# Kernel optimization log

Hardware: AMD Instinct MI355X
Metric: run time of the kernel (lower is better)

## Reference

```python
import jax, jax.numpy as jnp
import numpy as np

K = 5  # kernel_size per dim (dim=2 -> 25 kernels), B-spline degree 1, open spline


def spline_conv(x, edge_index, pseudo, W, root, bias):
    # x: [N, Cin], pseudo: [E, 2] in [0,1], W: [K*K, Cin, Cout]
    N = x.shape[0]
    src, dst = edge_index[0], edge_index[1]
    # Transform node features with every kernel weight once: [N, K*K, Cout]
    xk = jnp.einsum('ni,kio->nko', x, W)
    # Degree-1 open B-spline basis: v = u*(K-1); frac/1-frac weights over 2 knots per dim
    v = pseudo * (K - 1)
    bot = jnp.floor(v)
    frac = v - bot
    bot = bot.astype(jnp.int32)
    msg = jnp.zeros((src.shape[0], W.shape[2]), dtype=x.dtype)
    for s0 in (0, 1):
        for s1 in (0, 1):
            b0 = frac[:, 0] if s0 else (1.0 - frac[:, 0])
            b1 = frac[:, 1] if s1 else (1.0 - frac[:, 1])
            basis = b0 * b1  # [E]
            idx = (jnp.clip(bot[:, 0] + s0, 0, K - 1)
                   + K * jnp.clip(bot[:, 1] + s1, 0, K - 1))  # [E]
            msg = msg + basis[:, None] * xk[src, idx]  # gather [E, Cout]
    # scatter-max aggregation into target nodes; empty nodes -> 0 (PyG convention)
    agg = jax.ops.segment_max(msg, dst, num_segments=N)
    agg = jnp.where(jnp.isfinite(agg), agg, jnp.zeros_like(agg))
    return agg + x @ root + bias


def setup_inputs() -> dict:
    key = jax.random.key(0)
    ks = jax.random.split(key, 8)
    N, E, C = 50000, 1600000, 64
    Cin = C
    s = 1.0 / np.sqrt(25 * Cin)
    return {
        'x': jax.random.normal(ks[0], (N, C), dtype=jnp.float32),
        'edge_index': jax.random.randint(ks[1], (2, E), 0, N, dtype=jnp.int32),
        'edge_attr': jax.random.uniform(ks[2], (E, 2), dtype=jnp.float32),
        'W1': jax.random.normal(ks[3], (25, C, C), dtype=jnp.float32) * s,
        'root1': jax.random.normal(ks[4], (C, C), dtype=jnp.float32) / np.sqrt(C),
        'bias1': jnp.zeros((C,), dtype=jnp.float32),
        'W2': jax.random.normal(ks[5], (25, C, C), dtype=jnp.float32) * s,
        'root2': jax.random.normal(ks[6], (C, C), dtype=jnp.float32) / np.sqrt(C),
        'bias2': jnp.zeros((C,), dtype=jnp.float32),
    }


def reference(x, edge_index, edge_attr, W1, root1, bias1, W2, root2, bias2):
    h = jax.nn.relu(spline_conv(x, edge_index, edge_attr, W1, root1, bias1))
    out = spline_conv(h, edge_index, edge_attr, W2, root2, bias2)
    return out
```

## Files before the change

### kernel.cpp

```cpp
#include <hip/hip_runtime.h>
#include <hip/hip_bf16.h>
#include <math.h>

#define CHANNELS 64
#define KK 25
#define NBLK 26
#define NCOL (NBLK * CHANNELS)
#define NTILES (NCOL / 16)
#define ROWP 2560
#define GROUP_TILES 8
#define GROUP_BYTES (GROUP_TILES * 2048)
#define NGROUPS (NTILES / GROUP_TILES)
#define G_SPLIT 5

typedef __attribute__((ext_vector_type(8))) short bf16x8;
typedef __attribute__((ext_vector_type(4))) float f32x4;
typedef __attribute__((ext_vector_type(2))) float f32x2;
typedef unsigned int u32;

__device__ __forceinline__ u32 f2bfu(float f) {
    u32 u = __float_as_uint(f);
    return (u + 0x7FFFu + ((u >> 16) & 1u)) >> 16;
}
__device__ __forceinline__ short f2bf(float f) { return (short)f2bfu(f); }

__device__ __forceinline__ void async_copy16(const void* g, void* l) {
    __builtin_amdgcn_global_load_lds(
        (const __attribute__((address_space(1))) u32*)g,
        (__attribute__((address_space(3))) u32*)l, 16, 0, 0);
}

template<int N> struct IC { static constexpr int v = N; };
template<int G, int GEND, class F>
__device__ __forceinline__ void unrollg(F f) {
    if constexpr (G < GEND) { f(IC<G>{}); unrollg<G + 1, GEND>(f); }
}

__device__ constexpr int cell_stores(int c) {
    return (c < KK) ? (((c % 5) != 0) ? 4 : 0) : 4;
}
__device__ constexpr int grp_stores(int g) {
    return cell_stores(2 * g) + cell_stores(2 * g + 1);
}


__global__ __launch_bounds__(256) void scan_a(const u32* __restrict__ counts,
                                              u32* __restrict__ bsum, int N) {
    const int t = threadIdx.x;
    const int base = blockIdx.x * 1024 + t * 4;
    uint4 v = make_uint4(0, 0, 0, 0);
    if (base + 3 < N) v = *(const uint4*)(counts + base);
    else {
        if (base < N)     v.x = counts[base];
        if (base + 1 < N) v.y = counts[base + 1];
        if (base + 2 < N) v.z = counts[base + 2];
    }
    u32 s = v.x + v.y + v.z + v.w;
    for (int off = 32; off; off >>= 1) s += __shfl_down(s, off, 64);
    __shared__ u32 red[4];
    if ((t & 63) == 0) red[t >> 6] = s;
    __syncthreads();
    if (t == 0) bsum[blockIdx.x] = red[0] + red[1] + red[2] + red[3];
}

__global__ __launch_bounds__(64) void scan_b(u32* __restrict__ bsum, int nb) {
    const int lane = threadIdx.x;
    u32 run = 0;
    for (int base = 0; base < nb; base += 64) {
        u32 v = (base + lane < nb) ? bsum[base + lane] : 0u;
        const u32 orig = v;
        for (int off = 1; off < 64; off <<= 1) {
            u32 u = __shfl_up(v, off, 64);
            if (lane >= off) v += u;
        }
        if (base + lane < nb) bsum[base + lane] = run + v - orig;
        run += __shfl(v, 63, 64);
    }
}

__global__ __launch_bounds__(256) void scan_c(const u32* __restrict__ counts,
                                              const u32* __restrict__ bsum,
                                              u32* __restrict__ cursor, int N) {
    const int t = threadIdx.x;
    const int base = blockIdx.x * 1024 + t * 4;
    uint4 v = make_uint4(0, 0, 0, 0);
    if (base + 3 < N) v = *(const uint4*)(counts + base);
    else {
        if (base < N)     v.x = counts[base];
        if (base + 1 < N) v.y = counts[base + 1];
        if (base + 2 < N) v.z = counts[base + 2];
    }
    __shared__ u32 ps[256];
    ps[t] = v.x + v.y + v.z + v.w;
    __syncthreads();
    for (int off = 1; off < 256; off <<= 1) {
        u32 u = (t >= off) ? ps[t - off] : 0u;
        __syncthreads();
        ps[t] += u;
        __syncthreads();
    }
    u32 ex = ((t > 0) ? ps[t - 1] : 0u) + bsum[blockIdx.x];
    if (base < N)     cursor[base]     = ex;
    if (base + 1 < N) cursor[base + 1] = ex + v.x;
    if (base + 2 < N) cursor[base + 2] = ex + v.x + v.y;
    if (base + 3 < N) cursor[base + 3] = ex + v.x + v.y + v.z;
    if (base <= N - 1 && N - 1 <= base + 3)
        cursor[N] = ex + v.x + v.y + v.z + v.w;
}


__global__ __launch_bounds__(256) void prep_w(const float* __restrict__ W,
                                              const float* __restrict__ root,
                                              __hip_bfloat16* __restrict__ Wb) {
    int idx = blockIdx.x * 256 + threadIdx.x;
    if (idx >= NTILES * 2 * 64 * 8) return;
    int j = idx & 7;
    int l = (idx >> 3) & 63;
    int q = (idx >> 9) & 1;
    int t = idx >> 10;
    int cell = t >> 2;
    int o    = 4 * (l & 15) + (t & 3);
    int k    = q * 32 + (l >> 4) * 8 + j;
    float src = (cell < KK) ? W[cell * 4096 + k * 64 + o] : root[k * 64 + o];
    ((unsigned short*)Wb)[idx] = (unsigned short)f2bf(src);
}

template<int GR0, int GR1>
__device__ __forceinline__ void gemm_body(
    const float* __restrict__ X, const __hip_bfloat16* __restrict__ Wb,
    char* __restrict__ XK, float* __restrict__ rootf, int N)
{
    static_assert((2 * GR0) % 5 == 0 || 2 * GR0 >= KK, "prevp chain crosses kernel split");
    __shared__ __align__(16) char lds[2][GROUP_BYTES];
    const int lane = threadIdx.x & 63;
    const int wv   = threadIdx.x >> 6;
    const int rb   = blockIdx.x * 64 + wv * 16;
    const int m    = lane & 15;
    const int quad = lane >> 4;
    const int Nm1  = N - 1;

    const int rowc = min(rb + m, Nm1);
    const float* __restrict__ xp = X + (size_t)rowc * CHANNELS + quad * 8;
    float af[16];
    *(float4*)(af)      = *(const float4*)(xp);
    *(float4*)(af + 4)  = *(const float4*)(xp + 4);
    *(float4*)(af + 8)  = *(const float4*)(xp + 32);
    *(float4*)(af + 12) = *(const float4*)(xp + 36);
    bf16x8 A0, A1;
#pragma unroll
    for (int j = 0; j < 8; ++j) { A0[j] = f2bf(af[j]); A1[j] = f2bf(af[8 + j]); }

    const int r0 = rb + quad * 4;
    const char* __restrict__ wbc = (const char*)Wb;

    auto stage = [&](int gg, int buf) {
        const char* gsrc = wbc + (size_t)gg * GROUP_BYTES + wv * 4096 + lane * 16;
        char* lbase = lds[buf] + wv * 4096;
        async_copy16(gsrc,        lbase);
        async_copy16(gsrc + 1024, lbase + 1024);
        async_copy16(gsrc + 2048, lbase + 2048);
        async_copy16(gsrc + 3072, lbase + 3072);
    };

    u32 prevp[4] = {0u, 0u, 0u, 0u};

    stage(GR0, 0);

    unrollg<GR0, GR1>([&](auto icg) {
        constexpr int g = decltype(icg)::v;
        constexpr int K = (g == GR0) ? 0 : grp_stores(g - 1);
        asm volatile("s_waitcnt vmcnt(%0)" :: "i"(K) : "memory");
        asm volatile("s_waitcnt lgkmcnt(0)" ::: "memory");
        __builtin_amdgcn_s_barrier();
        __builtin_amdgcn_sched_barrier(0);
        if constexpr (g + 1 < GR1) stage(g + 1, (g + 1 - GR0) & 1);
        __builtin_amdgcn_sched_barrier(0);
        const char* lb = lds[(g - GR0) & 1] + lane * 16;

        auto cell = [&](auto ick, const char* cb) {
            constexpr int kc = decltype(ick)::v;
            f32x4 acc0 = {0.f, 0.f, 0.f, 0.f};
            f32x4 acc1 = {0.f, 0.f, 0.f, 0.f};
            f32x4 acc2 = {0.f, 0.f, 0.f, 0.f};
            f32x4 acc3 = {0.f, 0.f, 0.f, 0.f};
            acc0 = __builtin_amdgcn_mfma_f32_16x16x32_bf16(A0, *(const bf16x8*)(cb),        acc0, 0, 0, 0);
            acc0 = __builtin_amdgcn_mfma_f32_16x16x32_bf16(A1, *(const bf16x8*)(cb + 1024), acc0, 0, 0, 0);
            acc1 = __builtin_amdgcn_mfma_f32_16x16x32_bf16(A0, *(const bf16x8*)(cb + 2048), acc1, 0, 0, 0);
            acc1 = __builtin_amdgcn_mfma_f32_16x16x32_bf16(A1, *(const bf16x8*)(cb + 3072), acc1, 0, 0, 0);
            acc2 = __builtin_amdgcn_mfma_f32_16x16x32_bf16(A0, *(const bf16x8*)(cb + 4096), acc2, 0, 0, 0);
            acc2 = __builtin_amdgcn_mfma_f32_16x16x32_bf16(A1, *(const bf16x8*)(cb + 5120), acc2, 0, 0, 0);
            acc3 = __builtin_amdgcn_mfma_f32_16x16x32_bf16(A0, *(const bf16x8*)(cb + 6144), acc3, 0, 0, 0);
            acc3 = __builtin_amdgcn_mfma_f32_16x16x32_bf16(A1, *(const bf16x8*)(cb + 7168), acc3, 0, 0, 0);
            if constexpr (kc < KK) {
                constexpr int d1 = kc / 5;
                constexpr int d0 = kc % 5;
                u32 pk[4];
#pragma unroll
                for (int i = 0; i < 4; ++i) {
                    u32 p = __builtin_amdgcn_cvt_pk_fp8_f32(acc0[i], acc1[i], 0u, false);
                    p = __builtin_amdgcn_cvt_pk_fp8_f32(acc2[i], acc3[i], p, true);
                    pk[i] = p;
                }
                if constexpr (d0 >= 1) {
#pragma unroll
                    for (int i = 0; i < 4; ++i) {
                        const int r = min(r0 + i, Nm1);
                        *(uint2*)(XK + (size_t)r * ROWP
                                  + (d1 * 512 + (d0 - 1) * 128) + 8 * m) =
                            make_uint2(prevp[i], pk[i]);
                    }
                }
#pragma unroll
                for (int i = 0; i < 4; ++i) prevp[i] = pk[i];
            } else {
#pragma unroll
                for (int i = 0; i < 4; ++i) {
                    const int r = min(r0 + i, Nm1);
                    *(float4*)(rootf + (size_t)r * CHANNELS + 4 * m) =
                        make_float4(acc0[i], acc1[i], acc2[i], acc3[i]);
                }
            }
        };
        cell(IC<2 * g>{},     lb);
        cell(IC<2 * g + 1>{}, lb + 8192);
    });
}

__global__ __launch_bounds__(256) void gemm_hist(
    const float* __restrict__ X, const __hip_bfloat16* __restrict__ Wb,
    char* __restrict__ XK, float* __restrict__ rootf, int N, int gemm_blocks,
    const int* __restrict__ ei, u32* __restrict__ counts,
    u32* __restrict__ rank, int E)
{
    if ((int)blockIdx.x >= gemm_blocks) {
        const int e0 = ((int)blockIdx.x - gemm_blocks) * 1024 + threadIdx.x * 4;
        if (e0 + 3 < E) {
            const int4 d = *(const int4*)(ei + E + e0);
            const u32 r0 = atomicAdd(&counts[d.x], 1u);
            const u32 r1 = atomicAdd(&counts[d.y], 1u);
            const u32 r2 = atomicAdd(&counts[d.z], 1u);
            const u32 r3 = atomicAdd(&counts[d.w], 1u);
            *(uint4*)(rank + e0) = make_uint4(r0, r1, r2, r3);
        } else {
            for (int k = 0; k < 4; ++k)
                if (e0 + k < E)
                    rank[e0 + k] = atomicAdd(&counts[ei[E + e0 + k]], 1u);
        }
        return;
    }
    gemm_body<0, G_SPLIT>(X, Wb, XK, rootf, N);
}

__device__ __forceinline__ uint2 mkrec(int src, float v0f, float v1f) {
    const float v0 = v0f * 4.0f, v1 = v1f * 4.0f;
    const int p0 = max(min((int)floorf(v0), 3), 0);
    const int p1 = max(min((int)floorf(v1), 3), 0);
    const float f0 = v0 - (float)p0;
    const float f1 = v1 - (float)p1;
    const u32 f0q = min((u32)(f0 * 65536.0f), 65535u);
    const u32 f1q = min((u32)(f1 * 65536.0f), 65535u);
    uint2 rec;
    rec.x = (u32)src | ((u32)p0 << 16) | ((u32)p1 << 19);
    rec.y = f0q | (f1q << 16);
    return rec;
}

__global__ __launch_bounds__(256) void gemm_scatter(
    const float* __restrict__ X, const __hip_bfloat16* __restrict__ Wb,
    char* __restrict__ XK, float* __restrict__ rootf, int N, int gemm_blocks,
    const int* __restrict__ ei, const float* __restrict__ ps,
    const u32* __restrict__ rank, const u32* __restrict__ cursor,
    uint2* __restrict__ sorted, int E)
{
    if ((int)blockIdx.x >= gemm_blocks) {
        const int e0 = ((int)blockIdx.x - gemm_blocks) * 1024 + threadIdx.x * 4;
        if (e0 + 3 < E) {
            const int4 s  = *(const int4*)(ei + e0);
            const int4 d  = *(const int4*)(ei + E + e0);
            const float4 pa = *(const float4*)(ps + 2 * e0);
            const float4 pb = *(const float4*)(ps + 2 * e0 + 4);
            const uint4 rk = *(const uint4*)(rank + e0);
            const u32 c0 = cursor[d.x];
            const u32 c1 = cursor[d.y];
            const u32 c2 = cursor[d.z];
            const u32 c3 = cursor[d.w];
            sorted[c0 + rk.x] = mkrec(s.x, pa.x, pa.y);
            sorted[c1 + rk.y] = mkrec(s.y, pa.z, pa.w);
            sorted[c2 + rk.z] = mkrec(s.z, pb.x, pb.y);
            sorted[c3 + rk.w] = mkrec(s.w, pb.z, pb.w);
        } else {
            for (int k = 0; k < 4; ++k) {
                const int e = e0 + k;
                if (e < E)
                    sorted[cursor[ei[E + e]] + rank[e]] =
                        mkrec(ei[e], ps[2 * e], ps[2 * e + 1]);
            }
        }
        return;
    }
    gemm_body<G_SPLIT, NGROUPS>(X, Wb, XK, rootf, N);
}

__global__ __launch_bounds__(256) void gemm_only(
    const float* __restrict__ X, const __hip_bfloat16* __restrict__ Wb,
    char* __restrict__ XK, float* __restrict__ rootf, int N)
{
    gemm_body<0, NGROUPS>(X, Wb, XK, rootf, N);
}

__global__ __launch_bounds__(256) void agg_node_p(
    const uint2* __restrict__ sorted, const u32* __restrict__ cursor,
    const char* __restrict__ XK, const float* __restrict__ rootf,
    const float* __restrict__ bias, float* __restrict__ out, int N, int relu,
    int node_blocks, const float* __restrict__ Wsrc,
    const float* __restrict__ rootsrc, __hip_bfloat16* __restrict__ Wbdst)
{
    if ((int)blockIdx.x >= node_blocks) {
        int idx = ((int)blockIdx.x - node_blocks) * 256 + threadIdx.x;
        if (idx < NTILES * 2 * 64 * 8) {
            int j = idx & 7;
            int l = (idx >> 3) & 63;
            int q = (idx >> 9) & 1;
            int t = idx >> 10;
            int cell = t >> 2;
            int o    = 4 * (l & 15) + (t & 3);
            int k    = q * 32 + (l >> 4) * 8 + j;
            float s = (cell < KK) ? Wsrc[cell * 4096 + k * 64 + o] : rootsrc[k * 64 + o];
            ((unsigned short*)Wbdst)[idx] = (unsigned short)f2bf(s);
        }
        return;
    }
    const int lane = threadIdx.x & 63;
    const int n = blockIdx.x * 4 + (threadIdx.x >> 6);
    if (n >= N) return;
    const int q = lane >> 4, j = lane & 15;
    const int beg = (int)cursor[n];
    const int end = (int)cursor[n + 1];

    float m0 = -INFINITY, m1 = -INFINITY, m2 = -INFINITY, m3 = -INFINITY;
    if (beg < end) {
        const int last = end - 1;
#define GATHP(r, q0, q1)                                                       \
        {                                                                      \
            const char* b_ = XK + (size_t)((r).x & 0xffff) * ROWP + (j << 3);  \
            const int o_ = (((int)((r).x >> 16) & 7)                           \
                            + (((int)((r).x >> 19) & 7) << 2)) << 7;           \
            q0 = *(const uint2*)(b_ + o_);                                     \
            q1 = *(const uint2*)(b_ + o_ + 512);                               \
        }
        uint2 rA = sorted[min(beg + q,      last)];
        uint2 rB = sorted[min(beg + 4 + q,  last)];
        uint2 rC = sorted[min(beg + 8 + q,  last)];
        uint2 ga0, ga1, gb0, gb1, gc0, gc1;
        GATHP(rA, ga0, ga1)
        GATHP(rB, gb0, gb1)
        for (int i = beg; i < end; i += 4) {
            uint2 rD = sorted[min(i + 12 + q, last)];
            GATHP(rC, gc0, gc1)
            const float f0 = (float)(rA.y & 0xffff) * (1.0f / 65536.0f);
            const float f1 = (float)(rA.y >> 16)    * (1.0f / 65536.0f);
            const float w00 = (1.f - f0) * (1.f - f1);
            const float w10 = f0 * (1.f - f1);
            const float w01 = (1.f - f0) * f1;
            const float w11 = f0 * f1;
            f32x2 s01 = __builtin_amdgcn_cvt_pk_f32_fp8(ga0.x, false) * w00
                      + __builtin_amdgcn_cvt_pk_f32_fp8(ga0.y, false) * w10
                      + __builtin_amdgcn_cvt_pk_f32_fp8(ga1.x, false) * w01
                      + __builtin_amdgcn_cvt_pk_f32_fp8(ga1.y, false) * w11;
            f32x2 s23 = __builtin_amdgcn_cvt_pk_f32_fp8(ga0.x, true)  * w00
                      + __builtin_amdgcn_cvt_pk_f32_fp8(ga0.y, true)  * w10
                      + __builtin_amdgcn_cvt_pk_f32_fp8(ga1.x, true)  * w01
                      + __builtin_amdgcn_cvt_pk_f32_fp8(ga1.y, true)  * w11;
            m0 = fmaxf(m0, s01.x); m1 = fmaxf(m1, s01.y);
            m2 = fmaxf(m2, s23.x); m3 = fmaxf(m3, s23.y);
            rA = rB; rB = rC; rC = rD;
            ga0 = gb0; ga1 = gb1;
            gb0 = gc0; gb1 = gc1;
        }
#undef GATHP
    }
    m0 = fmaxf(m0, __shfl_xor(m0, 16, 64)); m0 = fmaxf(m0, __shfl_xor(m0, 32, 64));
    m1 = fmaxf(m1, __shfl_xor(m1, 16, 64)); m1 = fmaxf(m1, __shfl_xor(m1, 32, 64));
    m2 = fmaxf(m2, __shfl_xor(m2, 16, 64)); m2 = fmaxf(m2, __shfl_xor(m2, 32, 64));
    m3 = fmaxf(m3, __shfl_xor(m3, 16, 64)); m3 = fmaxf(m3, __shfl_xor(m3, 32, 64));
    const float a0 = isfinite(m0) ? m0 : 0.f;
    const float a1 = isfinite(m1) ? m1 : 0.f;
    const float a2 = isfinite(m2) ? m2 : 0.f;
    const float a3 = isfinite(m3) ? m3 : 0.f;

    const float4 rv = *(const float4*)(rootf + (size_t)n * CHANNELS + 4 * j);
    const float4 bv = *(const float4*)(bias + 4 * j);
    float r0 = a0 + rv.x + bv.x;
    float r1 = a1 + rv.y + bv.y;
    float r2 = a2 + rv.z + bv.z;
    float r3 = a3 + rv.w + bv.w;
    if (relu) {
        r0 = fmaxf(r0, 0.f); r1 = fmaxf(r1, 0.f);
        r2 = fmaxf(r2, 0.f); r3 = fmaxf(r3, 0.f);
    }
    if (q == 0)
        *(float4*)(out + (size_t)n * CHANNELS + 4 * j) = make_float4(r0, r1, r2, r3);
}

extern "C" void kernel_launch(void* const* d_in, const int* in_sizes, int n_in,
                              void* d_out, int out_size, void* d_ws, size_t ws_size,
                              hipStream_t stream) {
    const float* x     = (const float*)d_in[0];
    const int*   ei    = (const int*)d_in[1];
    const float* ps    = (const float*)d_in[2];
    const float* W1    = (const float*)d_in[3];
    const float* root1 = (const float*)d_in[4];
    const float* bias1 = (const float*)d_in[5];
    const float* W2    = (const float*)d_in[6];
    const float* root2 = (const float*)d_in[7];
    const float* bias2 = (const float*)d_in[8];
    float* out = (float*)d_out;

    const int N = in_sizes[0] / CHANNELS;
    const int E = in_sizes[1] / 2;

    char* ws = (char*)d_ws;
    char* xk = ws;
    size_t off = (size_t)N * ROWP;
    float* h = (float*)(ws + off);
    off += (size_t)N * CHANNELS * sizeof(float);
    float* rootf = (float*)(ws + off);
    off += (size_t)N * CHANNELS * sizeof(float);
    uint2* sorted = (uint2*)(ws + off);
    off += (size_t)E * sizeof(uint2);
    u32* rank = (u32*)(ws + off);
    off += (size_t)E * sizeof(u32);
    u32* counts = (u32*)(ws + off);
    off += (size_t)N * 4;
    __hip_bfloat16* Wb = (__hip_bfloat16*)(ws + off);
    off += (size_t)NTILES * 2 * 64 * 8 * 2;
    u32* cursor = (u32*)(ws + off);
    off += ((size_t)N + 1) * 4;
    u32* bsum = (u32*)(ws + off);

    const int prep_blocks = (NTILES * 2 * 64 * 8 + 255) / 256;
    const int gemm_blocks = (N + 63) / 64;
    const int node_blocks = (N + 3) / 4;
    const int edgeQ_blocks = (E + 1023) / 1024;
    const int scan_blocks = (N + 1023) / 1024;

    hipMemsetAsync(counts, 0, (size_t)N * 4, stream);
    prep_w<<<prep_blocks, 256, 0, stream>>>(W1, root1, Wb);

    gemm_hist<<<gemm_blocks + edgeQ_blocks, 256, 0, stream>>>(
        x, Wb, xk, rootf, N, gemm_blocks, ei, counts, rank, E);

    scan_a<<<scan_blocks, 256, 0, stream>>>(counts, bsum, N);
    scan_b<<<1, 64, 0, stream>>>(bsum, scan_blocks);
    scan_c<<<scan_blocks, 256, 0, stream>>>(counts, bsum, cursor, N);

    gemm_scatter<<<gemm_blocks + edgeQ_blocks, 256, 0, stream>>>(
        x, Wb, xk, rootf, N, gemm_blocks, ei, ps, rank, cursor, sorted, E);

    agg_node_p<<<node_blocks + prep_blocks, 256, 0, stream>>>(
        sorted, cursor, xk, rootf, bias1, h, N, 1, node_blocks, W2, root2, Wb);

    gemm_only<<<gemm_blocks, 256, 0, stream>>>(h, Wb, xk, rootf, N);
    agg_node_p<<<node_blocks, 256, 0, stream>>>(
        sorted, cursor, xk, rootf, bias2, out, N, 0, node_blocks, W2, root2, Wb);
}
```

Baseline: 416.6 us.

## Unfuse GEMM from edge sort, use atomic cursor scatter and nontemporal stores

The layer-1 GEMM is no longer split across the histogram and scatter kernels. It runs as its own kernel, with nontemporal stores for the transformed features. The histogram becomes a standalone kernel that only counts and no longer records per-edge ranks. The scatter now claims slots with atomic increments on a live copy of the cursor, which removes the rank array's write and read traffic. The cost is losing the overlap between edge sorting and GEMM, and the order of edges within each node becomes nondeterministic; that order is harmless for max aggregation.

```diff
diff --git a/kernel.cpp b/kernel.cpp
--- a/kernel.cpp
+++ b/kernel.cpp
@@ -11,12 +11,13 @@
 #define GROUP_TILES 8
 #define GROUP_BYTES (GROUP_TILES * 2048)
 #define NGROUPS (NTILES / GROUP_TILES)
-#define G_SPLIT 5
 
 typedef __attribute__((ext_vector_type(8))) short bf16x8;
 typedef __attribute__((ext_vector_type(4))) float f32x4;
 typedef __attribute__((ext_vector_type(2))) float f32x2;
 typedef unsigned int u32;
+typedef __attribute__((ext_vector_type(2))) unsigned int u32x2;
+typedef __attribute__((ext_vector_type(4))) float f32x4v;
 
 __device__ __forceinline__ u32 f2bfu(float f) {
     u32 u = __float_as_uint(f);
@@ -80,7 +81,8 @@
 
 __global__ __launch_bounds__(256) void scan_c(const u32* __restrict__ counts,
                                               const u32* __restrict__ bsum,
-                                              u32* __restrict__ cursor, int N) {
+                                              u32* __restrict__ cursor,
+                                              u32* __restrict__ curlive, int N) {
     const int t = threadIdx.x;
     const int base = blockIdx.x * 1024 + t * 4;
     uint4 v = make_uint4(0, 0, 0, 0);
@@ -100,12 +102,27 @@
         __syncthreads();
     }
     u32 ex = ((t > 0) ? ps[t - 1] : 0u) + bsum[blockIdx.x];
-    if (base < N)     cursor[base]     = ex;
-    if (base + 1 < N) cursor[base + 1] = ex + v.x;
-    if (base + 2 < N) cursor[base + 2] = ex + v.x + v.y;
-    if (base + 3 < N) cursor[base + 3] = ex + v.x + v.y + v.z;
+    if (base < N)     { cursor[base]     = ex;                   curlive[base]     = ex; }
+    if (base + 1 < N) { cursor[base + 1] = ex + v.x;             curlive[base + 1] = ex + v.x; }
+    if (base + 2 < N) { cursor[base + 2] = ex + v.x + v.y;       curlive[base + 2] = ex + v.x + v.y; }
+    if (base + 3 < N) { cursor[base + 3] = ex + v.x + v.y + v.z; curlive[base + 3] = ex + v.x + v.y + v.z; }
     if (base <= N - 1 && N - 1 <= base + 3)
         cursor[N] = ex + v.x + v.y + v.z + v.w;
+}
+
+__global__ __launch_bounds__(256) void hist_edges(const int* __restrict__ ei,
+                                                  u32* __restrict__ counts, int E) {
+    const int e0 = blockIdx.x * 1024 + threadIdx.x * 4;
+    if (e0 + 3 < E) {
+        const int4 d = *(const int4*)(ei + E + e0);
+        atomicAdd(&counts[d.x], 1u);
+        atomicAdd(&counts[d.y], 1u);
+        atomicAdd(&counts[d.z], 1u);
+        atomicAdd(&counts[d.w], 1u);
+    } else {
+        for (int k = 0; k < 4; ++k)
+            if (e0 + k < E) atomicAdd(&counts[ei[E + e0 + k]], 1u);
+    }
 }
 
 
@@ -125,12 +142,11 @@
     ((unsigned short*)Wb)[idx] = (unsigned short)f2bf(src);
 }
 
-template<int GR0, int GR1>
+template<int NT>
 __device__ __forceinline__ void gemm_body(
     const float* __restrict__ X, const __hip_bfloat16* __restrict__ Wb,
     char* __restrict__ XK, float* __restrict__ rootf, int N)
 {
-    static_assert((2 * GR0) % 5 == 0 || 2 * GR0 >= KK, "prevp chain crosses kernel split");
     __shared__ __align__(16) char lds[2][GROUP_BYTES];
     const int lane = threadIdx.x & 63;
     const int wv   = threadIdx.x >> 6;
@@ -164,18 +180,18 @@
 
     u32 prevp[4] = {0u, 0u, 0u, 0u};
 
-    stage(GR0, 0);
-
-    unrollg<GR0, GR1>([&](auto icg) {
+    stage(0, 0);
+
+    unrollg<0, NGROUPS>([&](auto icg) {
         constexpr int g = decltype(icg)::v;
-        constexpr int K = (g == GR0) ? 0 : grp_stores(g - 1);
+        constexpr int K = (g == 0) ? 0 : grp_stores(g - 1);
         asm volatile("s_waitcnt vmcnt(%0)" :: "i"(K) : "memory");
         asm volatile("s_waitcnt lgkmcnt(0)" ::: "memory");
         __builtin_amdgcn_s_barrier();
         __builtin_amdgcn_sched_barrier(0);
-        if constexpr (g + 1 < GR1) stage(g + 1, (g + 1 - GR0) & 1);
+        if constexpr (g + 1 < NGROUPS) stage(g + 1, (g + 1) & 1);
         __builtin_amdgcn_sched_barrier(0);
-        const char* lb = lds[(g - GR0) & 1] + lane * 16;
+        const char* lb = lds[g & 1] + lane * 16;
 
         auto cell = [&](auto ick, const char* cb) {
             constexpr int kc = decltype(ick)::v;
@@ -205,9 +221,14 @@
 #pragma unroll
                     for (int i = 0; i < 4; ++i) {
                         const int r = min(r0 + i, Nm1);
-                        *(uint2*)(XK + (size_t)r * ROWP
-                                  + (d1 * 512 + (d0 - 1) * 128) + 8 * m) =
-                            make_uint2(prevp[i], pk[i]);
+                        char* addr = XK + (size_t)r * ROWP
+                                     + (d1 * 512 + (d0 - 1) * 128) + 8 * m;
+                        if constexpr (NT) {
+                            u32x2 v; v.x = prevp[i]; v.y = pk[i];
+                            __builtin_nontemporal_store(v, (u32x2*)addr);
+                        } else {
+                            *(uint2*)addr = make_uint2(prevp[i], pk[i]);
+                        }
                     }
                 }
 #pragma unroll
@@ -216,8 +237,13 @@
 #pragma unroll
                 for (int i = 0; i < 4; ++i) {
                     const int r = min(r0 + i, Nm1);
-                    *(float4*)(rootf + (size_t)r * CHANNELS + 4 * m) =
-                        make_float4(acc0[i], acc1[i], acc2[i], acc3[i]);
+                    float* addr = rootf + (size_t)r * CHANNELS + 4 * m;
+                    if constexpr (NT) {
+                        f32x4v v; v.x = acc0[i]; v.y = acc1[i]; v.z = acc2[i]; v.w = acc3[i];
+                        __builtin_nontemporal_store(v, (f32x4v*)addr);
+                    } else {
+                        *(float4*)addr = make_float4(acc0[i], acc1[i], acc2[i], acc3[i]);
+                    }
                 }
             }
         };
@@ -226,29 +252,12 @@
     });
 }
 
-__global__ __launch_bounds__(256) void gemm_hist(
+template<int NT>
+__global__ __launch_bounds__(256) void gemm_only(
     const float* __restrict__ X, const __hip_bfloat16* __restrict__ Wb,
-    char* __restrict__ XK, float* __restrict__ rootf, int N, int gemm_blocks,
-    const int* __restrict__ ei, u32* __restrict__ counts,
-    u32* __restrict__ rank, int E)
+    char* __restrict__ XK, float* __restrict__ rootf, int N)
 {
-    if ((int)blockIdx.x >= gemm_blocks) {
-        const int e0 = ((int)blockIdx.x - gemm_blocks) * 1024 + threadIdx.x * 4;
-        if (e0 + 3 < E) {
-            const int4 d = *(const int4*)(ei + E + e0);
-            const u32 r0 = atomicAdd(&counts[d.x], 1u);
-            const u32 r1 = atomicAdd(&counts[d.y], 1u);
-            const u32 r2 = atomicAdd(&counts[d.z], 1u);
-            const u32 r3 = atomicAdd(&counts[d.w], 1u);
-            *(uint4*)(rank + e0) = make_uint4(r0, r1, r2, r3);
-        } else {
-            for (int k = 0; k < 4; ++k)
-                if (e0 + k < E)
-                    rank[e0 + k] = atomicAdd(&counts[ei[E + e0 + k]], 1u);
-        }
-        return;
-    }
-    gemm_body<0, G_SPLIT>(X, Wb, XK, rootf, N);
+    gemm_body<NT>(X, Wb, XK, rootf, N);
 }
 
 __device__ __forceinline__ uint2 mkrec(int src, float v0f, float v1f) {
@@ -265,47 +274,33 @@
     return rec;
 }
 
-__global__ __launch_bounds__(256) void gemm_scatter(
-    const float* __restrict__ X, const __hip_bfloat16* __restrict__ Wb,
-    char* __restrict__ XK, float* __restrict__ rootf, int N, int gemm_blocks,
+__global__ __launch_bounds__(256) void edge_scatter(
     const int* __restrict__ ei, const float* __restrict__ ps,
-    const u32* __restrict__ rank, const u32* __restrict__ cursor,
-    uint2* __restrict__ sorted, int E)
+    u32* __restrict__ curlive, uint2* __restrict__ sorted, int E)
 {
-    if ((int)blockIdx.x >= gemm_blocks) {
-        const int e0 = ((int)blockIdx.x - gemm_blocks) * 1024 + threadIdx.x * 4;
-        if (e0 + 3 < E) {
-            const int4 s  = *(const int4*)(ei + e0);
-            const int4 d  = *(const int4*)(ei + E + e0);
-            const float4 pa = *(const float4*)(ps + 2 * e0);
-            const float4 pb = *(const float4*)(ps + 2 * e0 + 4);
-            const uint4 rk = *(const uint4*)(rank + e0);
-            const u32 c0 = cursor[d.x];
-            const u32 c1 = cursor[d.y];
-            const u32 c2 = cursor[d.z];
-            const u32 c3 = cursor[d.w];
-            sorted[c0 + rk.x] = mkrec(s.x, pa.x, pa.y);
-            sorted[c1 + rk.y] = mkrec(s.y, pa.z, pa.w);
-            sorted[c2 + rk.z] = mkrec(s.z, pb.x, pb.y);
-            sorted[c3 + rk.w] = mkrec(s.w, pb.z, pb.w);
-        } else {
-            for (int k = 0; k < 4; ++k) {
-                const int e = e0 + k;
-                if (e < E)
-                    sorted[cursor[ei[E + e]] + rank[e]] =
-                        mkrec(ei[e], ps[2 * e], ps[2 * e + 1]);
+    const int e0 = blockIdx.x * 1024 + threadIdx.x * 4;
+    if (e0 + 3 < E) {
+        const int4 s  = *(const int4*)(ei + e0);
+        const int4 d  = *(const int4*)(ei + E + e0);
+        const float4 pa = *(const float4*)(ps + 2 * e0);
+        const float4 pb = *(const float4*)(ps + 2 * e0 + 4);
+        const u32 c0 = atomicAdd(&curlive[d.x], 1u);
+        const u32 c1 = atomicAdd(&curlive[d.y], 1u);
+        const u32 c2 = atomicAdd(&curlive[d.z], 1u);
+        const u32 c3 = atomicAdd(&curlive[d.w], 1u);
+        sorted[c0] = mkrec(s.x, pa.x, pa.y);
+        sorted[c1] = mkrec(s.y, pa.z, pa.w);
+        sorted[c2] = mkrec(s.z, pb.x, pb.y);
+        sorted[c3] = mkrec(s.w, pb.z, pb.w);
+    } else {
+        for (int k = 0; k < 4; ++k) {
+            const int e = e0 + k;
+            if (e < E) {
+                const u32 c = atomicAdd(&curlive[ei[E + e]], 1u);
+                sorted[c] = mkrec(ei[e], ps[2 * e], ps[2 * e + 1]);
             }
         }
-        return;
-    }
-    gemm_body<G_SPLIT, NGROUPS>(X, Wb, XK, rootf, N);
-}
-
-__global__ __launch_bounds__(256) void gemm_only(
-    const float* __restrict__ X, const __hip_bfloat16* __restrict__ Wb,
-    char* __restrict__ XK, float* __restrict__ rootf, int N)
-{
-    gemm_body<0, NGROUPS>(X, Wb, XK, rootf, N);
+    }
 }
 
 __global__ __launch_bounds__(256) void agg_node_p(
@@ -428,14 +423,14 @@
     off += (size_t)N * CHANNELS * sizeof(float);
     uint2* sorted = (uint2*)(ws + off);
     off += (size_t)E * sizeof(uint2);
-    u32* rank = (u32*)(ws + off);
-    off += (size_t)E * sizeof(u32);
     u32* counts = (u32*)(ws + off);
     off += (size_t)N * 4;
     __hip_bfloat16* Wb = (__hip_bfloat16*)(ws + off);
     off += (size_t)NTILES * 2 * 64 * 8 * 2;
     u32* cursor = (u32*)(ws + off);
     off += ((size_t)N + 1) * 4;
+    u32* curlive = (u32*)(ws + off);
+    off += ((size_t)N + 1) * 4;
     u32* bsum = (u32*)(ws + off);
 
     const int prep_blocks = (NTILES * 2 * 64 * 8 + 255) / 256;
@@ -445,22 +440,23 @@
     const int scan_blocks = (N + 1023) / 1024;
 
     hipMemsetAsync(counts, 0, (size_t)N * 4, stream);
+
+    hist_edges<<<edgeQ_blocks, 256, 0, stream>>>(ei, counts, E);
+
     prep_w<<<prep_blocks, 256, 0, stream>>>(W1, root1, Wb);
 
-    gemm_hist<<<gemm_blocks + edgeQ_blocks, 256, 0, stream>>>(
-        x, Wb, xk, rootf, N, gemm_blocks, ei, counts, rank, E);
+    gemm_only<1><<<gemm_blocks, 256, 0, stream>>>(x, Wb, xk, rootf, N);
 
     scan_a<<<scan_blocks, 256, 0, stream>>>(counts, bsum, N);
     scan_b<<<1, 64, 0, stream>>>(bsum, scan_blocks);
-    scan_c<<<scan_blocks, 256, 0, stream>>>(counts, bsum, cursor, N);
-
-    gemm_scatter<<<gemm_blocks + edgeQ_blocks, 256, 0, stream>>>(
-        x, Wb, xk, rootf, N, gemm_blocks, ei, ps, rank, cursor, sorted, E);
+    scan_c<<<scan_blocks, 256, 0, stream>>>(counts, bsum, cursor, curlive, N);
+
+    edge_scatter<<<edgeQ_blocks, 256, 0, stream>>>(ei, ps, curlive, sorted, E);
 
     agg_node_p<<<node_blocks + prep_blocks, 256, 0, stream>>>(
         sorted, cursor, xk, rootf, bias1, h, N, 1, node_blocks, W2, root2, Wb);
 
-    gemm_only<<<gemm_blocks, 256, 0, stream>>>(h, Wb, xk, rootf, N);
+    gemm_only<0><<<gemm_blocks, 256, 0, stream>>>(h, Wb, xk, rootf, N);
     agg_node_p<<<node_blocks, 256, 0, stream>>>(
         sorted, cursor, xk, rootf, bias2, out, N, 0, node_blocks, W2, root2, Wb);
 }
```

After: 476.4 us. +14.4%, slower.

## Use per-wave private weight staging in GEMM and unfuse edge passes

Applied to the files above, without the earlier changes.

The GEMM kernel now gives each wave its own double-buffered LDS copy of each 8 KB weight cell. This removes the block-wide s_barrier per group, and each wave prefetches two cells ahead using only vmcnt/lgkmcnt waits. The histogram and scatter edge passes are split back out of the fused GEMM launches into standalone kernels, and the GEMM runs as a single full kernel. The barriers go away, but each wave now loads the weights redundantly (4x the global-to-LDS traffic) and uses 64 KB of LDS per block, which may limit occupancy. Splitting the launches also loses the overlap between the edge work and the GEMM.

```diff
diff --git a/kernel.cpp b/kernel.cpp
--- a/kernel.cpp
+++ b/kernel.cpp
@@ -8,10 +8,7 @@
 #define NCOL (NBLK * CHANNELS)
 #define NTILES (NCOL / 16)
 #define ROWP 2560
-#define GROUP_TILES 8
-#define GROUP_BYTES (GROUP_TILES * 2048)
-#define NGROUPS (NTILES / GROUP_TILES)
-#define G_SPLIT 5
+#define CELL_BYTES 8192
 
 typedef __attribute__((ext_vector_type(8))) short bf16x8;
 typedef __attribute__((ext_vector_type(4))) float f32x4;
@@ -38,9 +35,6 @@
 
 __device__ constexpr int cell_stores(int c) {
     return (c < KK) ? (((c % 5) != 0) ? 4 : 0) : 4;
-}
-__device__ constexpr int grp_stores(int g) {
-    return cell_stores(2 * g) + cell_stores(2 * g + 1);
 }
 
 
@@ -106,6 +100,24 @@
     if (base + 3 < N) cursor[base + 3] = ex + v.x + v.y + v.z;
     if (base <= N - 1 && N - 1 <= base + 3)
         cursor[N] = ex + v.x + v.y + v.z + v.w;
+}
+
+__global__ __launch_bounds__(256) void hist_edges(const int* __restrict__ ei,
+                                                  u32* __restrict__ counts,
+                                                  u32* __restrict__ rank, int E) {
+    const int e0 = blockIdx.x * 1024 + threadIdx.x * 4;
+    if (e0 + 3 < E) {
+        const int4 d = *(const int4*)(ei + E + e0);
+        const u32 r0 = atomicAdd(&counts[d.x], 1u);
+        const u32 r1 = atomicAdd(&counts[d.y], 1u);
+        const u32 r2 = atomicAdd(&counts[d.z], 1u);
+        const u32 r3 = atomicAdd(&counts[d.w], 1u);
+        *(uint4*)(rank + e0) = make_uint4(r0, r1, r2, r3);
+    } else {
+        for (int k = 0; k < 4; ++k)
+            if (e0 + k < E)
+                rank[e0 + k] = atomicAdd(&counts[ei[E + e0 + k]], 1u);
+    }
 }
 
 
@@ -125,13 +137,11 @@
     ((unsigned short*)Wb)[idx] = (unsigned short)f2bf(src);
 }
 
-template<int GR0, int GR1>
-__device__ __forceinline__ void gemm_body(
+__global__ __launch_bounds__(256) void gemm_nb(
     const float* __restrict__ X, const __hip_bfloat16* __restrict__ Wb,
     char* __restrict__ XK, float* __restrict__ rootf, int N)
 {
-    static_assert((2 * GR0) % 5 == 0 || 2 * GR0 >= KK, "prevp chain crosses kernel split");
-    __shared__ __align__(16) char lds[2][GROUP_BYTES];
+    __shared__ __align__(16) char lds[4][2][CELL_BYTES];
     const int lane = threadIdx.x & 63;
     const int wv   = threadIdx.x >> 6;
     const int rb   = blockIdx.x * 64 + wv * 16;
@@ -152,103 +162,75 @@
 
     const int r0 = rb + quad * 4;
     const char* __restrict__ wbc = (const char*)Wb;
-
-    auto stage = [&](int gg, int buf) {
-        const char* gsrc = wbc + (size_t)gg * GROUP_BYTES + wv * 4096 + lane * 16;
-        char* lbase = lds[buf] + wv * 4096;
-        async_copy16(gsrc,        lbase);
-        async_copy16(gsrc + 1024, lbase + 1024);
-        async_copy16(gsrc + 2048, lbase + 2048);
-        async_copy16(gsrc + 3072, lbase + 3072);
+    char* const ldsw = &lds[wv][0][0];
+
+    auto stage = [&](int c, int buf) {
+        const char* gsrc = wbc + (size_t)c * CELL_BYTES + lane * 16;
+        char* lb = ldsw + buf * CELL_BYTES;
+#pragma unroll
+        for (int k = 0; k < 8; ++k)
+            async_copy16(gsrc + k * 1024, lb + k * 1024);
     };
 
     u32 prevp[4] = {0u, 0u, 0u, 0u};
 
-    stage(GR0, 0);
-
-    unrollg<GR0, GR1>([&](auto icg) {
-        constexpr int g = decltype(icg)::v;
-        constexpr int K = (g == GR0) ? 0 : grp_stores(g - 1);
-        asm volatile("s_waitcnt vmcnt(%0)" :: "i"(K) : "memory");
-        asm volatile("s_waitcnt lgkmcnt(0)" ::: "memory");
-        __builtin_amdgcn_s_barrier();
-        __builtin_amdgcn_sched_barrier(0);
-        if constexpr (g + 1 < GR1) stage(g + 1, (g + 1 - GR0) & 1);
-        __builtin_amdgcn_sched_barrier(0);
-        const char* lb = lds[(g - GR0) & 1] + lane * 16;
-
-        auto cell = [&](auto ick, const char* cb) {
-            constexpr int kc = decltype(ick)::v;
-            f32x4 acc0 = {0.f, 0.f, 0.f, 0.f};
-            f32x4 acc1 = {0.f, 0.f, 0.f, 0.f};
-            f32x4 acc2 = {0.f, 0.f, 0.f, 0.f};
-            f32x4 acc3 = {0.f, 0.f, 0.f, 0.f};
-            acc0 = __builtin_amdgcn_mfma_f32_16x16x32_bf16(A0, *(const bf16x8*)(cb),        acc0, 0, 0, 0);
-            acc0 = __builtin_amdgcn_mfma_f32_16x16x32_bf16(A1, *(const bf16x8*)(cb + 1024), acc0, 0, 0, 0);
-            acc1 = __builtin_amdgcn_mfma_f32_16x16x32_bf16(A0, *(const bf16x8*)(cb + 2048), acc1, 0, 0, 0);
-            acc1 = __builtin_amdgcn_mfma_f32_16x16x32_bf16(A1, *(const bf16x8*)(cb + 3072), acc1, 0, 0, 0);
-            acc2 = __builtin_amdgcn_mfma_f32_16x16x32_bf16(A0, *(const bf16x8*)(cb + 4096), acc2, 0, 0, 0);
-            acc2 = __builtin_amdgcn_mfma_f32_16x16x32_bf16(A1, *(const bf16x8*)(cb + 5120), acc2, 0, 0, 0);
-            acc3 = __builtin_amdgcn_mfma_f32_16x16x32_bf16(A0, *(const bf16x8*)(cb + 6144), acc3, 0, 0, 0);
-            acc3 = __builtin_amdgcn_mfma_f32_16x16x32_bf16(A1, *(const bf16x8*)(cb + 7168), acc3, 0, 0, 0);
-            if constexpr (kc < KK) {
-                constexpr int d1 = kc / 5;
-                constexpr int d0 = kc % 5;
-                u32 pk[4];
-#pragma unroll
-                for (int i = 0; i < 4; ++i) {
-                    u32 p = __builtin_amdgcn_cvt_pk_fp8_f32(acc0[i], acc1[i], 0u, false);
-                    p = __builtin_amdgcn_cvt_pk_fp8_f32(acc2[i], acc3[i], p, true);
-                    pk[i] = p;
-                }
-                if constexpr (d0 >= 1) {
-#pragma unroll
-                    for (int i = 0; i < 4; ++i) {
-                        const int r = min(r0 + i, Nm1);
-                        *(uint2*)(XK + (size_t)r * ROWP
-                                  + (d1 * 512 + (d0 - 1) * 128) + 8 * m) =
-                            make_uint2(prevp[i], pk[i]);
-                    }
-                }
-#pragma unroll
-                for (int i = 0; i < 4; ++i) prevp[i] = pk[i];
-            } else {
+    stage(0, 0);
+    stage(1, 1);
+
+    unrollg<0, NBLK>([&](auto icc) {
+        constexpr int c = decltype(icc)::v;
+        constexpr int NC = (c == 0) ? 8
+                         : cell_stores(c - 1) + ((c + 1 < NBLK) ? 8 : 0);
+        asm volatile("s_waitcnt vmcnt(%0)" :: "i"(NC) : "memory");
+
+        const char* cb = ldsw + (c & 1) * CELL_BYTES + lane * 16;
+        f32x4 acc0 = {0.f, 0.f, 0.f, 0.f};
+        f32x4 acc1 = {0.f, 0.f, 0.f, 0.f};
+        f32x4 acc2 = {0.f, 0.f, 0.f, 0.f};
+        f32x4 acc3 = {0.f, 0.f, 0.f, 0.f};
+        acc0 = __builtin_amdgcn_mfma_f32_16x16x32_bf16(A0, *(const bf16x8*)(cb),        acc0, 0, 0, 0);
+        acc0 = __builtin_amdgcn_mfma_f32_16x16x32_bf16(A1, *(const bf16x8*)(cb + 1024), acc0, 0, 0, 0);
+        acc1 = __builtin_amdgcn_mfma_f32_16x16x32_bf16(A0, *(const bf16x8*)(cb + 2048), acc1, 0, 0, 0);
+        acc1 = __builtin_amdgcn_mfma_f32_16x16x32_bf16(A1, *(const bf16x8*)(cb + 3072), acc1, 0, 0, 0);
+        acc2 = __builtin_amdgcn_mfma_f32_16x16x32_bf16(A0, *(const bf16x8*)(cb + 4096), acc2, 0, 0, 0);
+        acc2 = __builtin_amdgcn_mfma_f32_16x16x32_bf16(A1, *(const bf16x8*)(cb + 5120), acc2, 0, 0, 0);
+        acc3 = __builtin_amdgcn_mfma_f32_16x16x32_bf16(A0, *(const bf16x8*)(cb + 6144), acc3, 0, 0, 0);
+        acc3 = __builtin_amdgcn_mfma_f32_16x16x32_bf16(A1, *(const bf16x8*)(cb + 7168), acc3, 0, 0, 0);
+
+        if constexpr (c < KK) {
+            constexpr int d1 = c / 5;
+            constexpr int d0 = c % 5;
+            u32 pk[4];
+#pragma unroll
+            for (int i = 0; i < 4; ++i) {
+                u32 p = __builtin_amdgcn_cvt_pk_fp8_f32(acc0[i], acc1[i], 0u, false);
+                p = __builtin_amdgcn_cvt_pk_fp8_f32(acc2[i], acc3[i], p, true);
+                pk[i] = p;
+            }
+            if constexpr (d0 >= 1) {
 #pragma unroll
                 for (int i = 0; i < 4; ++i) {
                     const int r = min(r0 + i, Nm1);
-                    *(float4*)(rootf + (size_t)r * CHANNELS + 4 * m) =
-                        make_float4(acc0[i], acc1[i], acc2[i], acc3[i]);
+                    *(uint2*)(XK + (size_t)r * ROWP
+                              + (d1 * 512 + (d0 - 1) * 128) + 8 * m) =
+                        make_uint2(prevp[i], pk[i]);
                 }
             }
-        };
-        cell(IC<2 * g>{},     lb);
-        cell(IC<2 * g + 1>{}, lb + 8192);
+#pragma unroll
+            for (int i = 0; i < 4; ++i) prevp[i] = pk[i];
+        } else {
+#pragma unroll
+            for (int i = 0; i < 4; ++i) {
+                const int r = min(r0 + i, Nm1);
+                *(float4*)(rootf + (size_t)r * CHANNELS + 4 * m) =
+                    make_float4(acc0[i], acc1[i], acc2[i], acc3[i]);
+            }
+        }
+        if constexpr (c + 2 < NBLK) {
+            asm volatile("s_waitcnt lgkmcnt(0)" ::: "memory");
+            stage(c + 2, c & 1);
+        }
     });
-}
-
-__global__ __launch_bounds__(256) void gemm_hist(
-    const float* __restrict__ X, const __hip_bfloat16* __restrict__ Wb,
-    char* __restrict__ XK, float* __restrict__ rootf, int N, int gemm_blocks,
-    const int* __restrict__ ei, u32* __restrict__ counts,
-    u32* __restrict__ rank, int E)
-{
-    if ((int)blockIdx.x >= gemm_blocks) {
-        const int e0 = ((int)blockIdx.x - gemm_blocks) * 1024 + threadIdx.x * 4;
-        if (e0 + 3 < E) {
-            const int4 d = *(const int4*)(ei + E + e0);
-            const u32 r0 = atomicAdd(&counts[d.x], 1u);
-            const u32 r1 = atomicAdd(&counts[d.y], 1u);
-            const u32 r2 = atomicAdd(&counts[d.z], 1u);
-            const u32 r3 = atomicAdd(&counts[d.w], 1u);
-            *(uint4*)(rank + e0) = make_uint4(r0, r1, r2, r3);
-        } else {
-            for (int k = 0; k < 4; ++k)
-                if (e0 + k < E)
-                    rank[e0 + k] = atomicAdd(&counts[ei[E + e0 + k]], 1u);
-        }
-        return;
-    }
-    gemm_body<0, G_SPLIT>(X, Wb, XK, rootf, N);
 }
 
 __device__ __forceinline__ uint2 mkrec(int src, float v0f, float v1f) {
@@ -265,47 +247,34 @@
     return rec;
 }
 
-__global__ __launch_bounds__(256) void gemm_scatter(
-    const float* __restrict__ X, const __hip_bfloat16* __restrict__ Wb,
-    char* __restrict__ XK, float* __restrict__ rootf, int N, int gemm_blocks,
+__global__ __launch_bounds__(256) void edge_scatter(
     const int* __restrict__ ei, const float* __restrict__ ps,
     const u32* __restrict__ rank, const u32* __restrict__ cursor,
     uint2* __restrict__ sorted, int E)
 {
-    if ((int)blockIdx.x >= gemm_blocks) {
-        const int e0 = ((int)blockIdx.x - gemm_blocks) * 1024 + threadIdx.x * 4;
-        if (e0 + 3 < E) {
-            const int4 s  = *(const int4*)(ei + e0);
-            const int4 d  = *(const int4*)(ei + E + e0);
-            const float4 pa = *(const float4*)(ps + 2 * e0);
-            const float4 pb = *(const float4*)(ps + 2 * e0 + 4);
-            const uint4 rk = *(const uint4*)(rank + e0);
-            const u32 c0 = cursor[d.x];
-            const u32 c1 = cursor[d.y];
-            const u32 c2 = cursor[d.z];
-            const u32 c3 = cursor[d.w];
-            sorted[c0 + rk.x] = mkrec(s.x, pa.x, pa.y);
-            sorted[c1 + rk.y] = mkrec(s.y, pa.z, pa.w);
-            sorted[c2 + rk.z] = mkrec(s.z, pb.x, pb.y);
-            sorted[c3 + rk.w] = mkrec(s.w, pb.z, pb.w);
-        } else {
-            for (int k = 0; k < 4; ++k) {
-                const int e = e0 + k;
-                if (e < E)
-                    sorted[cursor[ei[E + e]] + rank[e]] =
-                        mkrec(ei[e], ps[2 * e], ps[2 * e + 1]);
-            }
-        }
-        return;
-    }
-    gemm_body<G_SPLIT, NGROUPS>(X, Wb, XK, rootf, N);
-}
-
-__global__ __launch_bounds__(256) void gemm_only(
-    const float* __restrict__ X, const __hip_bfloat16* __restrict__ Wb,
-    char* __restrict__ XK, float* __restrict__ rootf, int N)
-{
-    gemm_body<0, NGROUPS>(X, Wb, XK, rootf, N);
+    const int e0 = blockIdx.x * 1024 + threadIdx.x * 4;
+    if (e0 + 3 < E) {
+        const int4 s  = *(const int4*)(ei + e0);
+        const int4 d  = *(const int4*)(ei + E + e0);
+        const float4 pa = *(const float4*)(ps + 2 * e0);
+        const float4 pb = *(const float4*)(ps + 2 * e0 + 4);
+        const uint4 rk = *(const uint4*)(rank + e0);
+        const u32 c0 = cursor[d.x];
+        const u32 c1 = cursor[d.y];
+        const u32 c2 = cursor[d.z];
+        const u32 c3 = cursor[d.w];
+        sorted[c0 + rk.x] = mkrec(s.x, pa.x, pa.y);
+        sorted[c1 + rk.y] = mkrec(s.y, pa.z, pa.w);
+        sorted[c2 + rk.z] = mkrec(s.z, pb.x, pb.y);
+        sorted[c3 + rk.w] = mkrec(s.w, pb.z, pb.w);
+    } else {
+        for (int k = 0; k < 4; ++k) {
+            const int e = e0 + k;
+            if (e < E)
+                sorted[cursor[ei[E + e]] + rank[e]] =
+                    mkrec(ei[e], ps[2 * e], ps[2 * e + 1]);
+        }
+    }
 }
 
 __global__ __launch_bounds__(256) void agg_node_p(
@@ -447,20 +416,20 @@
     hipMemsetAsync(counts, 0, (size_t)N * 4, stream);
     prep_w<<<prep_blocks, 256, 0, stream>>>(W1, root1, Wb);
 
-    gemm_hist<<<gemm_blocks + edgeQ_blocks, 256, 0, stream>>>(
-        x, Wb, xk, rootf, N, gemm_blocks, ei, counts, rank, E);
+    hist_edges<<<edgeQ_blocks, 256, 0, stream>>>(ei, counts, rank, E);
+
+    gemm_nb<<<gemm_blocks, 256, 0, stream>>>(x, Wb, xk, rootf, N);
 
     scan_a<<<scan_blocks, 256, 0, stream>>>(counts, bsum, N);
     scan_b<<<1, 64, 0, stream>>>(bsum, scan_blocks);
     scan_c<<<scan_blocks, 256, 0, stream>>>(counts, bsum, cursor, N);
 
-    gemm_scatter<<<gemm_blocks + edgeQ_blocks, 256, 0, stream>>>(
-        x, Wb, xk, rootf, N, gemm_blocks, ei, ps, rank, cursor, sorted, E);
+    edge_scatter<<<edgeQ_blocks, 256, 0, stream>>>(ei, ps, rank, cursor, sorted, E);
 
     agg_node_p<<<node_blocks + prep_blocks, 256, 0, stream>>>(
         sorted, cursor, xk, rootf, bias1, h, N, 1, node_blocks, W2, root2, Wb);
 
-    gemm_only<<<gemm_blocks, 256, 0, stream>>>(h, Wb, xk, rootf, N);
+    gemm_nb<<<gemm_blocks, 256, 0, stream>>>(h, Wb, xk, rootf, N);
     agg_node_p<<<node_blocks, 256, 0, stream>>>(
         sorted, cursor, xk, rootf, bias2, out, N, 0, node_blocks, W2, root2, Wb);
 }
```

Result: no change. 413.7 us (-0.7%).
